# Optimization experiments

Measured on AMD Instinct MI355X. Metric: run time of the kernel, lower is better.

## Reference

```python
import jax, jax.numpy as jnp
import numpy as np

N_NODES = 100000
N_EDGES = 3200000
R0, R1, R2, N1 = 16, 8, 16, 32


def setup_inputs() -> dict:
    key = jax.random.key(0)
    ks = jax.random.split(key, 12)
    x = jax.random.normal(ks[0], (N_NODES, R0), dtype=jnp.float32)
    edge_index = jax.random.randint(ks[1], (2, N_EDGES), 0, N_NODES, dtype=jnp.int64)
    s = 0.1
    return {
        "x": x,
        "edge_index": edge_index,
        # GraphConv 1: lin_rel (weight+bias) applied to aggregated neighbors, lin_root (no bias) to self
        "W_rel1": jax.random.normal(ks[2], (R0, R1), dtype=jnp.float32) * s,
        "b_rel1": jnp.zeros((R1,), dtype=jnp.float32),
        "W_root1": jax.random.normal(ks[3], (R0, R1), dtype=jnp.float32) * s,
        # GraphConv 2
        "W_rel2": jax.random.normal(ks[4], (R1, R2), dtype=jnp.float32) * s,
        "b_rel2": jnp.zeros((R2,), dtype=jnp.float32),
        "W_root2": jax.random.normal(ks[5], (R1, R2), dtype=jnp.float32) * s,
        # fc layers
        "W_fc1": jax.random.normal(ks[6], (R2, N1), dtype=jnp.float32) * s,
        "b_fc1": jnp.zeros((N1,), dtype=jnp.float32),
        "W_fc2": jax.random.normal(ks[7], (N1, 1), dtype=jnp.float32) * s,
        "b_fc2": jnp.zeros((1,), dtype=jnp.float32),
    }


def _graph_conv(x, src, dst, W_rel, b_rel, W_root):
    # GraphConv with aggr='add': out_i = lin_rel(sum_{j->i} x_j) + lin_root(x_i)
    agg = jax.ops.segment_sum(x[src], dst, num_segments=N_NODES)  # [N, d_in]
    return agg @ W_rel + b_rel + x @ W_root


def reference(x, edge_index,
              W_rel1, b_rel1, W_root1,
              W_rel2, b_rel2, W_root2,
              W_fc1, b_fc1, W_fc2, b_fc2):
    src, dst = edge_index[0], edge_index[1]
    h = jax.nn.relu(_graph_conv(x, src, dst, W_rel1, b_rel1, W_root1))
    h = jax.nn.relu(_graph_conv(h, src, dst, W_rel2, b_rel2, W_root2))
    h = jax.nn.relu(h @ W_fc1 + b_fc1)
    out = h @ W_fc2 + b_fc2  # [N, 1]
    return out - jnp.mean(out)
```

## Files before the change

### kernel.cpp

```cpp
#include <hip/hip_runtime.h>

#define NN 100000
#define NE 3200000
#define BSH 7
#define BNODES 128
#define NBUCK 782
#define BCAP 4800
#define BIN_CHUNK 8192
#define NBIN_BLOCKS ((NE + BIN_CHUNK - 1) / BIN_CHUNK)
#define NL1_BLOCKS ((NN + 1023) / 1024)
#define SUB_BLOCKS 64
#define SUB_RANGE ((NN + SUB_BLOCKS - 1) / SUB_BLOCKS)

#define S1 2097152.0f
#define S2 524288.0f
#define INV_S1 (1.0f / S1)
#define INV_S2 (1.0f / S2)

__global__ void init_ws(int* __restrict__ p) {
    int t = threadIdx.x;
    if (t < NBUCK + 2) p[t] = 0;
}

struct BinSh {
    int stage[BIN_CHUNK];
    int hist[NBUCK];
    int loff[NBUCK + 1];
    int gbase[NBUCK];
    int psum[1024];
};
struct L1Sh { float sW[128], sR[128], sb[8]; };
union K1Sh { BinSh bin; L1Sh a; };

__global__ __launch_bounds__(1024) void layer1_bin(
    const float* __restrict__ x,
    const int* __restrict__ src, const int* __restrict__ dst,
    const float* __restrict__ Wrel1, const float* __restrict__ brel1,
    const float* __restrict__ Wroot1,
    int* __restrict__ y1q, int* __restrict__ initq,
    int* __restrict__ bucketCnt, int* __restrict__ bpay)
{
    __shared__ K1Sh sh;
    int t = threadIdx.x;
    int blk = blockIdx.x;

    if (blk >= NBIN_BLOCKS) {
        if (t < 128) { sh.a.sW[t] = Wrel1[t]; sh.a.sR[t] = Wroot1[t]; }
        if (t < 8)   sh.a.sb[t] = brel1[t];
        __syncthreads();
        int i = (blk - NBIN_BLOCKS) * 1024 + t;
        if (i >= NN) return;
        const float4* xp = (const float4*)(x + (size_t)i * 16);
        float4 x0 = xp[0], x1 = xp[1], x2 = xp[2], x3 = xp[3];
        float xi[16] = {x0.x, x0.y, x0.z, x0.w, x1.x, x1.y, x1.z, x1.w,
                        x2.x, x2.y, x2.z, x2.w, x3.x, x3.y, x3.z, x3.w};
        float y[8], r[8];
#pragma unroll
        for (int j = 0; j < 8; ++j) { y[j] = 0.0f; r[j] = sh.a.sb[j]; }
#pragma unroll
        for (int k = 0; k < 16; ++k) {
            float xv = xi[k];
#pragma unroll
            for (int j = 0; j < 8; ++j) {
                y[j] = fmaf(xv, sh.a.sW[k * 8 + j], y[j]);
                r[j] = fmaf(xv, sh.a.sR[k * 8 + j], r[j]);
            }
        }
        int4* yp = (int4*)(y1q + (size_t)i * 8);
        int4* ap = (int4*)(initq + (size_t)i * 8);
        int4 q0, q1, p0, p1;
        q0.x = __float2int_rn(y[0] * S1); q0.y = __float2int_rn(y[1] * S1);
        q0.z = __float2int_rn(y[2] * S1); q0.w = __float2int_rn(y[3] * S1);
        q1.x = __float2int_rn(y[4] * S1); q1.y = __float2int_rn(y[5] * S1);
        q1.z = __float2int_rn(y[6] * S1); q1.w = __float2int_rn(y[7] * S1);
        p0.x = __float2int_rn(r[0] * S1); p0.y = __float2int_rn(r[1] * S1);
        p0.z = __float2int_rn(r[2] * S1); p0.w = __float2int_rn(r[3] * S1);
        p1.x = __float2int_rn(r[4] * S1); p1.y = __float2int_rn(r[5] * S1);
        p1.z = __float2int_rn(r[6] * S1); p1.w = __float2int_rn(r[7] * S1);
        yp[0] = q0; yp[1] = q1;
        ap[0] = p0; ap[1] = p1;
        return;
    }

    int e0 = blk * BIN_CHUNK;
    int nE = NE - e0; if (nE > BIN_CHUNK) nE = BIN_CHUNK;
    int nv = nE >> 2;

    if (t < NBUCK) sh.bin.hist[t] = 0;
    __syncthreads();

    const int4* dst4 = (const int4*)(dst + e0);
    const int4* src4 = (const int4*)(src + e0);

    for (int k = t; k < nv; k += 1024) {
        int4 d4 = dst4[k];
        atomicAdd(&sh.bin.hist[d4.x >> BSH], 1);
        atomicAdd(&sh.bin.hist[d4.y >> BSH], 1);
        atomicAdd(&sh.bin.hist[d4.z >> BSH], 1);
        atomicAdd(&sh.bin.hist[d4.w >> BSH], 1);
    }
    __syncthreads();

    int c = (t < NBUCK) ? sh.bin.hist[t] : 0;
    sh.bin.psum[t] = c;
    __syncthreads();
    for (int off = 1; off < 1024; off <<= 1) {
        int u = (t >= off) ? sh.bin.psum[t - off] : 0;
        __syncthreads();
        sh.bin.psum[t] += u;
        __syncthreads();
    }
    if (t < NBUCK) sh.bin.loff[t] = sh.bin.psum[t] - c;
    if (t == 0) sh.bin.loff[NBUCK] = nE;
    __syncthreads();

    if (t < NBUCK) {
        sh.bin.gbase[t] = c ? atomicAdd(&bucketCnt[t], c) : 0;
        sh.bin.hist[t] = sh.bin.loff[t];
    }
    __syncthreads();

    for (int k = t; k < nv; k += 1024) {
        int4 d4 = dst4[k];
        int4 s4 = src4[k];
        int b, r;
        b = d4.x >> BSH; r = atomicAdd(&sh.bin.hist[b], 1);
        sh.bin.stage[r] = ((d4.x & (BNODES - 1)) << 17) | s4.x;
        b = d4.y >> BSH; r = atomicAdd(&sh.bin.hist[b], 1);
        sh.bin.stage[r] = ((d4.y & (BNODES - 1)) << 17) | s4.y;
        b = d4.z >> BSH; r = atomicAdd(&sh.bin.hist[b], 1);
        sh.bin.stage[r] = ((d4.z & (BNODES - 1)) << 17) | s4.z;
        b = d4.w >> BSH; r = atomicAdd(&sh.bin.hist[b], 1);
        sh.bin.stage[r] = ((d4.w & (BNODES - 1)) << 17) | s4.w;
    }
    __syncthreads();

    for (int p = t; p < nE; p += 1024) {
        int lo = 0, hi = NBUCK - 1;
        while (lo < hi) {
            int mid = (lo + hi + 1) >> 1;
            if (sh.bin.loff[mid] <= p) lo = mid; else hi = mid - 1;
        }
        int ob = sh.bin.gbase[lo] + (p - sh.bin.loff[lo]);
        if (ob < BCAP) bpay[lo * BCAP + ob] = sh.bin.stage[p];
    }
}

__global__ __launch_bounds__(512, 8) void bucket_agg1(const int* __restrict__ bucketCnt,
                                                      const int* __restrict__ bpay,
                                                      const int* __restrict__ y1q,
                                                      int* __restrict__ h1q ) {
    __shared__ int4 sidx4[BCAP / 4];
    __shared__ int qacc[BNODES * 8];
    int t = threadIdx.x;
    int b = blockIdx.x;
    int gb = b * BCAP;
    int fbase = b * (BNODES * 8);

    int C = bucketCnt[b]; if (C > BCAP) C = BCAP;
    const int4* bp4 = (const int4*)(bpay + gb);
    int C4 = (C + 3) >> 2;
    for (int k = t; k < C4; k += 512) sidx4[k] = bp4[k];
    for (int k = t; k < BNODES * 8; k += 512) {
        int gi = fbase + k;
        qacc[k] = (gi < NN * 8) ? h1q[gi] : 0;
    }
    __syncthreads();

    int f = t & 7, g = t >> 3;
    const int* sidx = (const int*)sidx4;
    int full = C >> 9;
    for (int it = 0; it < full; ++it) {
        int base4 = (it << 7) + (g << 1);
        int4 va = sidx4[base4];
        int4 vb = sidx4[base4 + 1];
        int a0 = y1q[((va.x & 0x1FFFF) << 3) + f];
        int a1 = y1q[((va.y & 0x1FFFF) << 3) + f];
        int a2 = y1q[((va.z & 0x1FFFF) << 3) + f];
        int a3 = y1q[((va.w & 0x1FFFF) << 3) + f];
        int a4 = y1q[((vb.x & 0x1FFFF) << 3) + f];
        int a5 = y1q[((vb.y & 0x1FFFF) << 3) + f];
        int a6 = y1q[((vb.z & 0x1FFFF) << 3) + f];
        int a7 = y1q[((vb.w & 0x1FFFF) << 3) + f];
        atomicAdd(&qacc[((va.x >> 17) << 3) + f], a0);
        atomicAdd(&qacc[((va.y >> 17) << 3) + f], a1);
        atomicAdd(&qacc[((va.z >> 17) << 3) + f], a2);
        atomicAdd(&qacc[((va.w >> 17) << 3) + f], a3);
        atomicAdd(&qacc[((vb.x >> 17) << 3) + f], a4);
        atomicAdd(&qacc[((vb.y >> 17) << 3) + f], a5);
        atomicAdd(&qacc[((vb.z >> 17) << 3) + f], a6);
        atomicAdd(&qacc[((vb.w >> 17) << 3) + f], a7);
    }
    for (int e = (full << 9) + g; e < C; e += 64) {
        int v = sidx[e];
        int a = y1q[((v & 0x1FFFF) << 3) + f];
        atomicAdd(&qacc[((v >> 17) << 3) + f], a);
    }
    __syncthreads();

    for (int k = t; k < BNODES * 8; k += 512) {
        int gi = fbase + k;
        if (gi < NN * 8) {
            float h = (float)qacc[k] * INV_S1;
            h = h > 0.0f ? h : 0.0f;
            h1q[gi] = __float2int_rn(h * S2);
        }
    }
}

__global__ __launch_bounds__(512, 8) void bucket_agg2_tail_sub(
    const int* __restrict__ bucketCnt,
    const int* __restrict__ bpay,
    const int* __restrict__ h1q,
    const float* __restrict__ Wrel2, const float* __restrict__ brel2,
    const float* __restrict__ Wroot2,
    const float* __restrict__ Wfc1, const float* __restrict__ bfc1,
    const float* __restrict__ Wfc2, const float* __restrict__ bfc2,
    float* __restrict__ out, float* __restrict__ gsum, int* __restrict__ done)
{
    __shared__ int4 sidx4[BCAP / 4];
    __shared__ int qacc[BNODES * 8];
    __shared__ float sWrel2[128], sWroot2[128], sbrel2[16];
    __shared__ float sWfc1[512], sbfc1[32], sWfc2[32];
    __shared__ float sbfc2;
    __shared__ float wsum[8];
    __shared__ int sticket;

    int t = threadIdx.x;
    int b = blockIdx.x;
    int gb = b * BCAP;
    int n0 = b * BNODES;

    int C = bucketCnt[b]; if (C > BCAP) C = BCAP;
    const int4* bp4 = (const int4*)(bpay + gb);
    int C4 = (C + 3) >> 2;
    for (int k = t; k < C4; k += 512) sidx4[k] = bp4[k];
    for (int k = t; k < BNODES * 8; k += 512) qacc[k] = 0;
    sWfc1[t] = Wfc1[t];
    if (t < 128) { sWrel2[t] = Wrel2[t]; sWroot2[t] = Wroot2[t]; }
    if (t >= 128 && t < 144) sbrel2[t - 128] = brel2[t - 128];
    if (t >= 192 && t < 224) { sbfc1[t - 192] = bfc1[t - 192]; sWfc2[t - 192] = Wfc2[t - 192]; }
    if (t == 256) sbfc2 = bfc2[0];
    __syncthreads();

    int f = t & 7, g = t >> 3;
    const int* sidx = (const int*)sidx4;
    int full = C >> 9;
    for (int it = 0; it < full; ++it) {
        int base4 = (it << 7) + (g << 1);
        int4 va = sidx4[base4];
        int4 vb = sidx4[base4 + 1];
        int a0 = h1q[((va.x & 0x1FFFF) << 3) + f];
        int a1 = h1q[((va.y & 0x1FFFF) << 3) + f];
        int a2 = h1q[((va.z & 0x1FFFF) << 3) + f];
        int a3 = h1q[((va.w & 0x1FFFF) << 3) + f];
        int a4 = h1q[((vb.x & 0x1FFFF) << 3) + f];
        int a5 = h1q[((vb.y & 0x1FFFF) << 3) + f];
        int a6 = h1q[((vb.z & 0x1FFFF) << 3) + f];
        int a7 = h1q[((vb.w & 0x1FFFF) << 3) + f];
        atomicAdd(&qacc[((va.x >> 17) << 3) + f], a0);
        atomicAdd(&qacc[((va.y >> 17) << 3) + f], a1);
        atomicAdd(&qacc[((va.z >> 17) << 3) + f], a2);
        atomicAdd(&qacc[((va.w >> 17) << 3) + f], a3);
        atomicAdd(&qacc[((vb.x >> 17) << 3) + f], a4);
        atomicAdd(&qacc[((vb.y >> 17) << 3) + f], a5);
        atomicAdd(&qacc[((vb.z >> 17) << 3) + f], a6);
        atomicAdd(&qacc[((vb.w >> 17) << 3) + f], a7);
    }
    for (int e = (full << 9) + g; e < C; e += 64) {
        int v = sidx[e];
        int a = h1q[((v & 0x1FFFF) << 3) + f];
        atomicAdd(&qacc[((v >> 17) << 3) + f], a);
    }
    __syncthreads();

    float o = 0.0f;
    int node = n0 + t;
    if (t < BNODES && node < NN) {
        const int4* hp = (const int4*)(h1q + (size_t)node * 8);
        int4 ha = hp[0], hb = hp[1];
        float h1v[8] = {ha.x * INV_S2, ha.y * INV_S2, ha.z * INV_S2, ha.w * INV_S2,
                        hb.x * INV_S2, hb.y * INV_S2, hb.z * INV_S2, hb.w * INV_S2};
        float s2[8];
#pragma unroll
        for (int j = 0; j < 8; ++j) s2[j] = (float)qacc[t * 8 + j] * INV_S2;

        float h2[16];
#pragma unroll
        for (int j = 0; j < 16; ++j) h2[j] = sbrel2[j];
#pragma unroll
        for (int k = 0; k < 8; ++k) {
            float sv = s2[k], hv = h1v[k];
#pragma unroll
            for (int j = 0; j < 16; ++j) {
                h2[j] = fmaf(sv, sWrel2[k * 16 + j], h2[j]);
                h2[j] = fmaf(hv, sWroot2[k * 16 + j], h2[j]);
            }
        }
#pragma unroll
        for (int j = 0; j < 16; ++j) h2[j] = h2[j] > 0.0f ? h2[j] : 0.0f;

        o = sbfc2;
#pragma unroll
        for (int m = 0; m < 32; ++m) {
            float a = sbfc1[m];
#pragma unroll
            for (int j = 0; j < 16; ++j) a = fmaf(h2[j], sWfc1[j * 32 + m], a);
            a = a > 0.0f ? a : 0.0f;
            o = fmaf(a, sWfc2[m], o);
        }
        out[node] = o;
    }

    float v = o;
#pragma unroll
    for (int off = 32; off > 0; off >>= 1) v += __shfl_down(v, off);
    int lane = t & 63, w = t >> 6;
    if (lane == 0) wsum[w] = v;
    __syncthreads();
    if (t == 0) {
        float s = 0.0f;
#pragma unroll
        for (int k = 0; k < 8; ++k) s += wsum[k];
        atomicAdd(gsum, s);
        __threadfence();
        sticket = atomicAdd(done, 1);
    }
    __syncthreads();

    int ticket = sticket;
    if (ticket < NBUCK - SUB_BLOCKS) return;

    if (t == 0) {
        while (__hip_atomic_load(done, __ATOMIC_ACQUIRE, __HIP_MEMORY_SCOPE_AGENT) < NBUCK) {}
    }
    __syncthreads();
    float m = __hip_atomic_load(gsum, __ATOMIC_RELAXED, __HIP_MEMORY_SCOPE_AGENT)
              * (1.0f / (float)NN);
    int r = ticket - (NBUCK - SUB_BLOCKS);
    int s0 = r * SUB_RANGE;
    int s1 = s0 + SUB_RANGE; if (s1 > NN) s1 = NN;
    for (int i = s0 + t; i < s1; i += 512) out[i] -= m;
}

extern "C" void kernel_launch(void* const* d_in, const int* in_sizes, int n_in,
                              void* d_out, int out_size, void* d_ws, size_t ws_size,
                              hipStream_t stream) {
    const float* x      = (const float*)d_in[0];
    const int*   ei     = (const int*)d_in[1];
    const float* Wrel1  = (const float*)d_in[2];
    const float* brel1  = (const float*)d_in[3];
    const float* Wroot1 = (const float*)d_in[4];
    const float* Wrel2  = (const float*)d_in[5];
    const float* brel2  = (const float*)d_in[6];
    const float* Wroot2 = (const float*)d_in[7];
    const float* Wfc1   = (const float*)d_in[8];
    const float* bfc1   = (const float*)d_in[9];
    const float* Wfc2   = (const float*)d_in[10];
    const float* bfc2   = (const float*)d_in[11];
    float* out = (float*)d_out;
    float* ws  = (float*)d_ws;

    int*   y1q       = (int*)ws;
    int*   h1q       = (int*)(ws + 800000);
    int*   bucketCnt = (int*)(ws + 1600000);
    float* gsum      = ws + 1600782;
    int*   done      = (int*)(ws + 1600783);
    int*   bpay      = (int*)(ws + 1600784);

    const int* src = ei;
    const int* dst = ei + NE;

    init_ws<<<1, 1024, 0, stream>>>(bucketCnt);
    layer1_bin<<<NBIN_BLOCKS + NL1_BLOCKS, 1024, 0, stream>>>(
        x, src, dst, Wrel1, brel1, Wroot1, y1q, h1q, bucketCnt, bpay);
    bucket_agg1<<<NBUCK, 512, 0, stream>>>(bucketCnt, bpay, y1q, h1q);
    bucket_agg2_tail_sub<<<NBUCK, 512, 0, stream>>>(bucketCnt, bpay, h1q,
                                                    Wrel2, brel2, Wroot2,
                                                    Wfc1, bfc1, Wfc2, bfc2,
                                                    out, gsum, done);
}
```

Baseline: 195.1 us.

## Vectorize gather to int4 per half-row and transpose shared accumulator layout

New measurement: 195.3 us. Within noise of the previous version (+0.1%).

```diff
diff --git a/kernel.cpp b/kernel.cpp
--- a/kernel.cpp
+++ b/kernel.cpp
@@ -146,7 +146,7 @@
     }
 }
 
-__global__ __launch_bounds__(512, 8) void bucket_agg1(const int* __restrict__ bucketCnt,
+__global__ __launch_bounds__(512, 4) void bucket_agg1(const int* __restrict__ bucketCnt,
                                                       const int* __restrict__ bpay,
                                                       const int* __restrict__ y1q,
                                                       int* __restrict__ h1q ) {
@@ -163,52 +163,59 @@
     for (int k = t; k < C4; k += 512) sidx4[k] = bp4[k];
     for (int k = t; k < BNODES * 8; k += 512) {
         int gi = fbase + k;
-        qacc[k] = (gi < NN * 8) ? h1q[gi] : 0;
-    }
-    __syncthreads();
-
-    int f = t & 7, g = t >> 3;
+        int v = (gi < NN * 8) ? h1q[gi] : 0;
+        qacc[(k & 7) * BNODES + (k >> 3)] = v;
+    }
+    __syncthreads();
+
     const int* sidx = (const int*)sidx4;
-    int full = C >> 9;
+    int h = t & 1;
+    int base = t >> 1;
+    int hq = h << 2;
+    int full = C >> 10;
     for (int it = 0; it < full; ++it) {
-        int base4 = (it << 7) + (g << 1);
-        int4 va = sidx4[base4];
-        int4 vb = sidx4[base4 + 1];
-        int a0 = y1q[((va.x & 0x1FFFF) << 3) + f];
-        int a1 = y1q[((va.y & 0x1FFFF) << 3) + f];
-        int a2 = y1q[((va.z & 0x1FFFF) << 3) + f];
-        int a3 = y1q[((va.w & 0x1FFFF) << 3) + f];
-        int a4 = y1q[((vb.x & 0x1FFFF) << 3) + f];
-        int a5 = y1q[((vb.y & 0x1FFFF) << 3) + f];
-        int a6 = y1q[((vb.z & 0x1FFFF) << 3) + f];
-        int a7 = y1q[((vb.w & 0x1FFFF) << 3) + f];
-        atomicAdd(&qacc[((va.x >> 17) << 3) + f], a0);
-        atomicAdd(&qacc[((va.y >> 17) << 3) + f], a1);
-        atomicAdd(&qacc[((va.z >> 17) << 3) + f], a2);
-        atomicAdd(&qacc[((va.w >> 17) << 3) + f], a3);
-        atomicAdd(&qacc[((vb.x >> 17) << 3) + f], a4);
-        atomicAdd(&qacc[((vb.y >> 17) << 3) + f], a5);
-        atomicAdd(&qacc[((vb.z >> 17) << 3) + f], a6);
-        atomicAdd(&qacc[((vb.w >> 17) << 3) + f], a7);
-    }
-    for (int e = (full << 9) + g; e < C; e += 64) {
+        int e0 = (it << 10) + base;
+        int v0 = sidx[e0];
+        int v1 = sidx[e0 + 256];
+        int v2 = sidx[e0 + 512];
+        int v3 = sidx[e0 + 768];
+        const int4 q0 = *(const int4*)(y1q + ((v0 & 0x1FFFF) << 3) + hq);
+        const int4 q1 = *(const int4*)(y1q + ((v1 & 0x1FFFF) << 3) + hq);
+        const int4 q2 = *(const int4*)(y1q + ((v2 & 0x1FFFF) << 3) + hq);
+        const int4 q3 = *(const int4*)(y1q + ((v3 & 0x1FFFF) << 3) + hq);
+        int d0 = (v0 >> 17) + hq * BNODES;
+        int d1 = (v1 >> 17) + hq * BNODES;
+        int d2 = (v2 >> 17) + hq * BNODES;
+        int d3 = (v3 >> 17) + hq * BNODES;
+        atomicAdd(&qacc[d0], q0.x); atomicAdd(&qacc[d0 + BNODES], q0.y);
+        atomicAdd(&qacc[d0 + 2 * BNODES], q0.z); atomicAdd(&qacc[d0 + 3 * BNODES], q0.w);
+        atomicAdd(&qacc[d1], q1.x); atomicAdd(&qacc[d1 + BNODES], q1.y);
+        atomicAdd(&qacc[d1 + 2 * BNODES], q1.z); atomicAdd(&qacc[d1 + 3 * BNODES], q1.w);
+        atomicAdd(&qacc[d2], q2.x); atomicAdd(&qacc[d2 + BNODES], q2.y);
+        atomicAdd(&qacc[d2 + 2 * BNODES], q2.z); atomicAdd(&qacc[d2 + 3 * BNODES], q2.w);
+        atomicAdd(&qacc[d3], q3.x); atomicAdd(&qacc[d3 + BNODES], q3.y);
+        atomicAdd(&qacc[d3 + 2 * BNODES], q3.z); atomicAdd(&qacc[d3 + 3 * BNODES], q3.w);
+    }
+    for (int e = (full << 10) + base; e < C; e += 256) {
         int v = sidx[e];
-        int a = y1q[((v & 0x1FFFF) << 3) + f];
-        atomicAdd(&qacc[((v >> 17) << 3) + f], a);
+        const int4 q = *(const int4*)(y1q + ((v & 0x1FFFF) << 3) + hq);
+        int d = (v >> 17) + hq * BNODES;
+        atomicAdd(&qacc[d], q.x); atomicAdd(&qacc[d + BNODES], q.y);
+        atomicAdd(&qacc[d + 2 * BNODES], q.z); atomicAdd(&qacc[d + 3 * BNODES], q.w);
     }
     __syncthreads();
 
     for (int k = t; k < BNODES * 8; k += 512) {
         int gi = fbase + k;
         if (gi < NN * 8) {
-            float h = (float)qacc[k] * INV_S1;
-            h = h > 0.0f ? h : 0.0f;
-            h1q[gi] = __float2int_rn(h * S2);
-        }
-    }
-}
-
-__global__ __launch_bounds__(512, 8) void bucket_agg2_tail_sub(
+            float hh = (float)qacc[(k & 7) * BNODES + (k >> 3)] * INV_S1;
+            hh = hh > 0.0f ? hh : 0.0f;
+            h1q[gi] = __float2int_rn(hh * S2);
+        }
+    }
+}
+
+__global__ __launch_bounds__(512, 4) void bucket_agg2_tail_sub(
     const int* __restrict__ bucketCnt,
     const int* __restrict__ bpay,
     const int* __restrict__ h1q,
@@ -243,34 +250,40 @@
     if (t == 256) sbfc2 = bfc2[0];
     __syncthreads();
 
-    int f = t & 7, g = t >> 3;
     const int* sidx = (const int*)sidx4;
-    int full = C >> 9;
+    int h = t & 1;
+    int base = t >> 1;
+    int hq = h << 2;
+    int full = C >> 10;
     for (int it = 0; it < full; ++it) {
-        int base4 = (it << 7) + (g << 1);
-        int4 va = sidx4[base4];
-        int4 vb = sidx4[base4 + 1];
-        int a0 = h1q[((va.x & 0x1FFFF) << 3) + f];
-        int a1 = h1q[((va.y & 0x1FFFF) << 3) + f];
-        int a2 = h1q[((va.z & 0x1FFFF) << 3) + f];
-        int a3 = h1q[((va.w & 0x1FFFF) << 3) + f];
-        int a4 = h1q[((vb.x & 0x1FFFF) << 3) + f];
-        int a5 = h1q[((vb.y & 0x1FFFF) << 3) + f];
-        int a6 = h1q[((vb.z & 0x1FFFF) << 3) + f];
-        int a7 = h1q[((vb.w & 0x1FFFF) << 3) + f];
-        atomicAdd(&qacc[((va.x >> 17) << 3) + f], a0);
-        atomicAdd(&qacc[((va.y >> 17) << 3) + f], a1);
-        atomicAdd(&qacc[((va.z >> 17) << 3) + f], a2);
-        atomicAdd(&qacc[((va.w >> 17) << 3) + f], a3);
-        atomicAdd(&qacc[((vb.x >> 17) << 3) + f], a4);
-        atomicAdd(&qacc[((vb.y >> 17) << 3) + f], a5);
-        atomicAdd(&qacc[((vb.z >> 17) << 3) + f], a6);
-        atomicAdd(&qacc[((vb.w >> 17) << 3) + f], a7);
-    }
-    for (int e = (full << 9) + g; e < C; e += 64) {
+        int e0 = (it << 10) + base;
+        int v0 = sidx[e0];
+        int v1 = sidx[e0 + 256];
+        int v2 = sidx[e0 + 512];
+        int v3 = sidx[e0 + 768];
+        const int4 q0 = *(const int4*)(h1q + ((v0 & 0x1FFFF) << 3) + hq);
+        const int4 q1 = *(const int4*)(h1q + ((v1 & 0x1FFFF) << 3) + hq);
+        const int4 q2 = *(const int4*)(h1q + ((v2 & 0x1FFFF) << 3) + hq);
+        const int4 q3 = *(const int4*)(h1q + ((v3 & 0x1FFFF) << 3) + hq);
+        int d0 = (v0 >> 17) + hq * BNODES;
+        int d1 = (v1 >> 17) + hq * BNODES;
+        int d2 = (v2 >> 17) + hq * BNODES;
+        int d3 = (v3 >> 17) + hq * BNODES;
+        atomicAdd(&qacc[d0], q0.x); atomicAdd(&qacc[d0 + BNODES], q0.y);
+        atomicAdd(&qacc[d0 + 2 * BNODES], q0.z); atomicAdd(&qacc[d0 + 3 * BNODES], q0.w);
+        atomicAdd(&qacc[d1], q1.x); atomicAdd(&qacc[d1 + BNODES], q1.y);
+        atomicAdd(&qacc[d1 + 2 * BNODES], q1.z); atomicAdd(&qacc[d1 + 3 * BNODES], q1.w);
+        atomicAdd(&qacc[d2], q2.x); atomicAdd(&qacc[d2 + BNODES], q2.y);
+        atomicAdd(&qacc[d2 + 2 * BNODES], q2.z); atomicAdd(&qacc[d2 + 3 * BNODES], q2.w);
+        atomicAdd(&qacc[d3], q3.x); atomicAdd(&qacc[d3 + BNODES], q3.y);
+        atomicAdd(&qacc[d3 + 2 * BNODES], q3.z); atomicAdd(&qacc[d3 + 3 * BNODES], q3.w);
+    }
+    for (int e = (full << 10) + base; e < C; e += 256) {
         int v = sidx[e];
-        int a = h1q[((v & 0x1FFFF) << 3) + f];
-        atomicAdd(&qacc[((v >> 17) << 3) + f], a);
+        const int4 q = *(const int4*)(h1q + ((v & 0x1FFFF) << 3) + hq);
+        int d = (v >> 17) + hq * BNODES;
+        atomicAdd(&qacc[d], q.x); atomicAdd(&qacc[d + BNODES], q.y);
+        atomicAdd(&qacc[d + 2 * BNODES], q.z); atomicAdd(&qacc[d + 3 * BNODES], q.w);
     }
     __syncthreads();
 
@@ -283,7 +296,7 @@
                         hb.x * INV_S2, hb.y * INV_S2, hb.z * INV_S2, hb.w * INV_S2};
         float s2[8];
 #pragma unroll
-        for (int j = 0; j < 8; ++j) s2[j] = (float)qacc[t * 8 + j] * INV_S2;
+        for (int j = 0; j < 8; ++j) s2[j] = (float)qacc[j * BNODES + t] * INV_S2;
 
         float h2[16];
 #pragma unroll
```
